# Optimization experiments

Hardware: AMD Instinct MI355X
Metric: run time of the kernel (lower is better)

## Reference

```python
import jax, jax.numpy as jnp
import numpy as np

N_NODES = 2048
D = 1024
B = 16384
E = 65536

def setup_inputs() -> dict:
    key = jax.random.key(0)
    ks = jax.random.split(key, 8)
    feat = jax.random.normal(ks[0], (B, 7, D), dtype=jnp.float32)
    data_x = jax.random.randint(ks[1], (7 * B,), 0, N_NODES, dtype=jnp.int64)
    adj_rows = jnp.sort(jax.random.randint(ks[2], (E,), 0, N_NODES, dtype=jnp.int32))
    adj_cols = jax.random.randint(ks[3], (E,), 0, N_NODES, dtype=jnp.int32)
    adj_vals = jax.random.uniform(ks[4], (E,), dtype=jnp.float32)
    # kaiming-uniform-like init for GCN weights, zero bias (as in reset_parameters)
    def kaiming(k, fan_in, fan_out):
        bound = jnp.sqrt(6.0 / fan_in)
        return jax.random.uniform(k, (fan_in, fan_out), minval=-bound, maxval=bound, dtype=jnp.float32)
    W1 = kaiming(ks[5], D, N_NODES)
    W2 = kaiming(ks[6], N_NODES, N_NODES)
    W3 = kaiming(ks[7], N_NODES, D)
    return {"feat": feat, "data_x": data_x, "adj_rows": adj_rows, "adj_cols": adj_cols,
            "adj_vals": adj_vals, "W1": W1, "b1": jnp.zeros((N_NODES,), jnp.float32),
            "W2": W2, "b2": jnp.zeros((N_NODES,), jnp.float32),
            "W3": W3, "b3": jnp.zeros((D,), jnp.float32)}

def reference(feat, data_x, adj_rows, adj_cols, adj_vals, W1, b1, W2, b2, W3, b3):
    n = b1.shape[0]  # number of nodes N
    e1 = data_x[0::7]  # [B]
    e2 = data_x[1::7]  # [B]
    # scatter-add: adjacency_matrix[e1] += feat[i,0]; adjacency_matrix[e2] += feat[i,1]
    idx = jnp.concatenate([e1, e2])                       # [2B]
    vals = jnp.concatenate([feat[:, 0, :], feat[:, 1, :]])  # [2B, D]
    node_feat = jax.ops.segment_sum(vals, idx, num_segments=n)  # [N, D]

    def spmm(x):  # sparse [N,N] @ dense [N,F]
        return jax.ops.segment_sum(adj_vals[:, None] * x[adj_cols], adj_rows, num_segments=n)

    h = jax.nn.relu(spmm(node_feat @ W1) + b1)  # [N, N]
    h = spmm(h @ W2) + b2                        # [N, N]
    logits = spmm(h @ W3) + b3                   # [N, D]

    # gather then swap: feat[:,0]=logits[e2], feat[:,1]=logits[e1]
    out = jnp.concatenate([logits[e2][:, None, :], logits[e1][:, None, :], feat[:, 2:, :]], axis=1)
    return out
```

## Files before the change

### kernel.cpp

```cpp
#include <hip/hip_runtime.h>
#include <stdint.h>

#define N_NODES 2048
#define DIM 1024
#define BATCH 16384
#define NEDGE 65536
#define CAP 96

typedef __bf16 bf16x8 __attribute__((ext_vector_type(8)));
typedef float f32x4 __attribute__((ext_vector_type(4)));
typedef unsigned short u16;
typedef unsigned int u32;

__device__ __forceinline__ float bf2f(u16 u) {
  union { u32 i; float f; } v; v.i = ((u32)u) << 16; return v.f;
}
__device__ __forceinline__ u16 f2bf(float f) {
  union { float f; u32 i; } v; v.f = f;
  u32 r = v.i + 0x7fffu + ((v.i >> 16) & 1u);
  return (u16)(r >> 16);
}

__global__ void k_detect(const int* __restrict__ dx, int* __restrict__ flag,
                         int* __restrict__ counts) {
  int t = threadIdx.x;
  for (int j = t; j < N_NODES; j += 64) counts[j] = 0;
  if (t == 0) {
    int is64 = 1;
    for (int j = 0; j < 32; ++j)
      if (dx[2 * j + 1] != 0) { is64 = 0; break; }
    *flag = is64;
  }
}

__global__ __launch_bounds__(256) void k_cvt(const int* __restrict__ dx,
                                             const int* __restrict__ flag,
                                             int* __restrict__ idx) {
  int i = blockIdx.x * 256 + threadIdx.x;
  if (i >= 7 * BATCH) return;
  int v = (*flag) ? dx[2 * i] : dx[i];
  idx[i] = v & (N_NODES - 1);
}

__global__ __launch_bounds__(256) void k_bucket(const int* __restrict__ idx,
                                                int* __restrict__ counts,
                                                int* __restrict__ bucket) {
  int i = blockIdx.x * 256 + threadIdx.x;
  if (i >= 2 * BATCH) return;
  int n = (i < BATCH) ? idx[7 * i] : idx[7 * (i - BATCH) + 1];
  int slot = atomicAdd(&counts[n], 1);
  if (slot < CAP) bucket[n * CAP + slot] = i;
}

__global__ __launch_bounds__(256) void k_nodesum(const float* __restrict__ feat,
                                                 const int* __restrict__ counts,
                                                 const int* __restrict__ bucket,
                                                 u16* __restrict__ A1) {
  int n = blockIdx.x;
  int tid = threadIdx.x;
  int cnt = counts[n]; if (cnt > CAP) cnt = CAP;
  float a0 = 0.f, a1 = 0.f, a2 = 0.f, a3 = 0.f;
  for (int j = 0; j < cnt; ++j) {
    int i = bucket[n * CAP + j];
    size_t rowoff = (i < BATCH) ? ((size_t)i * 7) * DIM
                                : ((size_t)(i - BATCH) * 7 + 1) * DIM;
    f32x4 v = *(const f32x4*)(feat + rowoff + tid * 4);
    a0 += v[0]; a1 += v[1]; a2 += v[2]; a3 += v[3];
  }
  ushort4 o; o.x = f2bf(a0); o.y = f2bf(a1); o.z = f2bf(a2); o.w = f2bf(a3);
  *(ushort4*)(A1 + (size_t)n * DIM + tid * 4) = o;
}

__global__ __launch_bounds__(256) void k_transpose(const float* __restrict__ W,
                                                   u16* __restrict__ Wt,
                                                   int K, int N) {
  __shared__ __align__(16) u16 t[32][33];
  int ntx = N >> 5;
  int bx = blockIdx.x % ntx;
  int by = blockIdx.x / ntx;
  int tx = threadIdx.x & 31, ty = threadIdx.x >> 5;
  #pragma unroll
  for (int r = 0; r < 32; r += 8)
    t[r + ty][tx] = f2bf(W[(size_t)(by * 32 + r + ty) * N + bx * 32 + tx]);
  __syncthreads();
  #pragma unroll
  for (int r = 0; r < 32; r += 8)
    Wt[(size_t)(bx * 32 + r + ty) * K + by * 32 + tx] = t[tx][r + ty];
}

__global__ __launch_bounds__(256) void k_rowptr(const int* __restrict__ adj_rows,
                                                int* __restrict__ row_ptr) {
  int r = blockIdx.x * 256 + threadIdx.x;
  if (r > N_NODES) return;
  int lo = 0, hi = NEDGE;
  while (lo < hi) { int mid = (lo + hi) >> 1; if (adj_rows[mid] < r) lo = mid + 1; else hi = mid; }
  row_ptr[r] = lo;
}

__global__ __launch_bounds__(256) void k_spmm(const u16* __restrict__ X16,
                                              const int* __restrict__ row_ptr,
                                              const int* __restrict__ adj_cols,
                                              const float* __restrict__ adj_vals,
                                              const float* __restrict__ bias,
                                              u16* __restrict__ Y16,
                                              float* __restrict__ Y32,
                                              int width) {
  int chunks = width >> 10;
  int ch = blockIdx.x % chunks;
  int r = blockIdx.x / chunks;
  int col = ch * 1024 + threadIdx.x * 4;
  int e0 = row_ptr[r], e1 = row_ptr[r + 1];
  float a0 = 0.f, a1 = 0.f, a2 = 0.f, a3 = 0.f;
  for (int e = e0; e < e1; ++e) {
    int c = adj_cols[e] & (N_NODES - 1);
    float v = adj_vals[e];
    ushort4 x = *(const ushort4*)(X16 + (size_t)c * width + col);
    a0 += v * bf2f(x.x); a1 += v * bf2f(x.y);
    a2 += v * bf2f(x.z); a3 += v * bf2f(x.w);
  }
  if (Y16) {
    ushort4 o; o.x = f2bf(a0); o.y = f2bf(a1); o.z = f2bf(a2); o.w = f2bf(a3);
    *(ushort4*)(Y16 + (size_t)r * width + col) = o;
  } else {
    f32x4 bb = *(const f32x4*)(bias + col);
    f32x4 o; o[0] = a0 + bb[0]; o[1] = a1 + bb[1]; o[2] = a2 + bb[2]; o[3] = a3 + bb[3];
    *(f32x4*)(Y32 + (size_t)r * width + col) = o;
  }
}

template <int BM, int BN, bool BIAS, bool RELU>
__global__ __launch_bounds__(256) void k_gemm(const u16* __restrict__ A,
                                              const u16* __restrict__ Bt,
                                              const float* __restrict__ bias,
                                              u16* __restrict__ C16,
                                              int M, int N, int K) {
  constexpr int WM = BM / 2, WN = BN / 2;
  constexpr int MI = WM / 16, NI = WN / 16;
  constexpr int IA = BM / 64, IB = BN / 64;
  __shared__ __align__(16) u16 As[BM * 32];
  __shared__ __align__(16) u16 Bs[BN * 32];
  const int ntx = N / BN;
  const int bx = blockIdx.x % ntx;
  const int by = blockIdx.x / ntx;
  const int tid = threadIdx.x;
  const int wid = tid >> 6;
  const int lane = tid & 63;
  const int wr = wid >> 1, wc = wid & 1;
  const int rowbase = by * BM, colbase = bx * BN;

  f32x4 acc[MI][NI];
  #pragma unroll
  for (int i = 0; i < MI; ++i)
    #pragma unroll
    for (int j = 0; j < NI; ++j) acc[i][j] = (f32x4){0.f, 0.f, 0.f, 0.f};

  const int srow = wid * 16 + (lane >> 2);
  const int skk = (lane & 3) * 8;

  for (int kt = 0; kt < K; kt += 32) {
    #pragma unroll
    for (int i = 0; i < IA; ++i) {
      const u16* g = A + (size_t)(rowbase + i * 64 + srow) * K + kt + skk;
      __builtin_amdgcn_global_load_lds(
          (const __attribute__((address_space(1))) u32*)g,
          (__attribute__((address_space(3))) u32*)(As + i * 2048 + wid * 512), 16, 0, 0);
    }
    #pragma unroll
    for (int i = 0; i < IB; ++i) {
      const u16* g = Bt + (size_t)(colbase + i * 64 + srow) * K + kt + skk;
      __builtin_amdgcn_global_load_lds(
          (const __attribute__((address_space(1))) u32*)g,
          (__attribute__((address_space(3))) u32*)(Bs + i * 2048 + wid * 512), 16, 0, 0);
    }
    __syncthreads();
    bf16x8 af[MI], bfr[NI];
    #pragma unroll
    for (int mi = 0; mi < MI; ++mi) {
      int row = wr * WM + mi * 16 + (lane & 15);
      af[mi] = *(const bf16x8*)(As + row * 32 + (lane >> 4) * 8);
    }
    #pragma unroll
    for (int ni = 0; ni < NI; ++ni) {
      int col = wc * WN + ni * 16 + (lane & 15);
      bfr[ni] = *(const bf16x8*)(Bs + col * 32 + (lane >> 4) * 8);
    }
    #pragma unroll
    for (int mi = 0; mi < MI; ++mi)
      #pragma unroll
      for (int ni = 0; ni < NI; ++ni)
        acc[mi][ni] = __builtin_amdgcn_mfma_f32_16x16x32_bf16(af[mi], bfr[ni], acc[mi][ni], 0, 0, 0);
    __syncthreads();
  }

  #pragma unroll
  for (int mi = 0; mi < MI; ++mi) {
    #pragma unroll
    for (int ni = 0; ni < NI; ++ni) {
      int col = colbase + wc * WN + ni * 16 + (lane & 15);
      float bv = BIAS ? bias[col] : 0.f;
      #pragma unroll
      for (int j = 0; j < 4; ++j) {
        int row = rowbase + wr * WM + mi * 16 + (lane >> 4) * 4 + j;
        float v = acc[mi][ni][j] + bv;
        if (RELU) v = fmaxf(v, 0.f);
        C16[(size_t)row * N + col] = f2bf(v);
      }
    }
  }
}

__global__ __launch_bounds__(256) void k_assemble(const float* __restrict__ feat,
                                                  const float* __restrict__ logits,
                                                  const int* __restrict__ idx,
                                                  float* __restrict__ out) {
  int i = blockIdx.x;
  int b = i / 7, slot = i - b * 7;
  const float* src;
  if (slot == 0)      src = logits + (size_t)idx[7 * b + 1] * DIM;
  else if (slot == 1) src = logits + (size_t)idx[7 * b] * DIM;
  else                src = feat + ((size_t)b * 7 + slot) * DIM;
  f32x4 v = *(const f32x4*)(src + threadIdx.x * 4);
  __builtin_nontemporal_store(v, (f32x4*)(out + ((size_t)b * 7 + slot) * DIM + threadIdx.x * 4));
}

extern "C" void kernel_launch(void* const* d_in, const int* in_sizes, int n_in,
                              void* d_out, int out_size, void* d_ws, size_t ws_size,
                              hipStream_t stream) {
  const float* feat   = (const float*)d_in[0];
  const int* data_x   = (const int*)d_in[1];
  const int* adj_rows = (const int*)d_in[2];
  const int* adj_cols = (const int*)d_in[3];
  const float* adj_vals = (const float*)d_in[4];
  const float* W1 = (const float*)d_in[5];
  const float* b1 = (const float*)d_in[6];
  const float* W2 = (const float*)d_in[7];
  const float* b2 = (const float*)d_in[8];
  const float* W3 = (const float*)d_in[9];
  const float* b3 = (const float*)d_in[10];
  float* out = (float*)d_out;

  char* ws = (char*)d_ws;
  size_t off = 0;
  auto alloc = [&](size_t bytes) {
    char* p = ws + off; off += (bytes + 511) & ~(size_t)511; return p;
  };
  int*  flag    = (int*)alloc(4);
  int*  idx32   = (int*)alloc((size_t)7 * BATCH * 4);
  int*  counts  = (int*)alloc(N_NODES * 4);
  int*  bucket  = (int*)alloc((size_t)N_NODES * CAP * 4);
  int*  row_ptr = (int*)alloc((N_NODES + 1) * 4);
  u16*  A1      = (u16*)alloc((size_t)N_NODES * DIM * 2);
  u16*  S       = (u16*)alloc((size_t)N_NODES * N_NODES * 2);
  u16*  H       = (u16*)alloc((size_t)N_NODES * N_NODES * 2);
  u16*  X3      = (u16*)alloc((size_t)N_NODES * DIM * 2);
  u16*  Wt      = (u16*)alloc((size_t)N_NODES * N_NODES * 2);
  float* logits = (float*)alloc((size_t)N_NODES * DIM * 4);

  k_detect<<<1, 64, 0, stream>>>(data_x, flag, counts);
  k_cvt<<<(7 * BATCH + 255) / 256, 256, 0, stream>>>(data_x, flag, idx32);
  k_bucket<<<(2 * BATCH + 255) / 256, 256, 0, stream>>>(idx32, counts, bucket);
  k_nodesum<<<N_NODES, 256, 0, stream>>>(feat, counts, bucket, A1);
  k_rowptr<<<N_NODES / 256 + 1, 256, 0, stream>>>(adj_rows, row_ptr);

  k_transpose<<<(N_NODES / 32) * (DIM / 32), 256, 0, stream>>>(W1, Wt, DIM, N_NODES);
  k_spmm<<<N_NODES * (DIM / 1024), 256, 0, stream>>>(A1, row_ptr, adj_cols, adj_vals, nullptr, S, nullptr, DIM);
  k_gemm<128, 64, true, true><<<(N_NODES / 128) * (N_NODES / 64), 256, 0, stream>>>(S, Wt, b1, H, N_NODES, N_NODES, DIM);
  k_transpose<<<(N_NODES / 32) * (N_NODES / 32), 256, 0, stream>>>(W2, Wt, N_NODES, N_NODES);
  k_spmm<<<N_NODES * (N_NODES / 1024), 256, 0, stream>>>(H, row_ptr, adj_cols, adj_vals, nullptr, S, nullptr, N_NODES);
  k_gemm<128, 64, true, false><<<(N_NODES / 128) * (N_NODES / 64), 256, 0, stream>>>(S, Wt, b2, H, N_NODES, N_NODES, N_NODES);
  k_transpose<<<(DIM / 32) * (N_NODES / 32), 256, 0, stream>>>(W3, Wt, N_NODES, DIM);
  k_gemm<64, 64, false, false><<<(N_NODES / 64) * (DIM / 64), 256, 0, stream>>>(H, Wt, nullptr, X3, N_NODES, DIM, N_NODES);
  k_spmm<<<N_NODES * (DIM / 1024), 256, 0, stream>>>(X3, row_ptr, adj_cols, adj_vals, b3, nullptr, logits, DIM);

  k_assemble<<<BATCH * 7, 256, 0, stream>>>(feat, logits, idx32, out);
}
```

Baseline: 354.1 us.

## Double-buffer GEMM with BK=64 swizzled LDS, unroll SpMM, drop index conversion kernel

The GEMM moves to a 64-wide K tile with double-buffered LDS, prefetching the next tile while MFMAs run on the current one. An XOR swizzle on LDS addresses is meant to avoid bank conflicts. The SpMM edge loop is unrolled by two so more gather loads are in flight at once. The separate index-conversion kernel is removed, and k_bucket and k_assemble now read data_x directly with the 64-bit flag, saving one launch and an intermediate buffer. The cost is doubled LDS use, which may reduce occupancy.

```diff
diff --git a/kernel.cpp b/kernel.cpp
--- a/kernel.cpp
+++ b/kernel.cpp
@@ -33,21 +33,15 @@
   }
 }
 
-__global__ __launch_bounds__(256) void k_cvt(const int* __restrict__ dx,
-                                             const int* __restrict__ flag,
-                                             int* __restrict__ idx) {
-  int i = blockIdx.x * 256 + threadIdx.x;
-  if (i >= 7 * BATCH) return;
-  int v = (*flag) ? dx[2 * i] : dx[i];
-  idx[i] = v & (N_NODES - 1);
-}
-
-__global__ __launch_bounds__(256) void k_bucket(const int* __restrict__ idx,
+__global__ __launch_bounds__(256) void k_bucket(const int* __restrict__ dx,
+                                                const int* __restrict__ flag,
                                                 int* __restrict__ counts,
                                                 int* __restrict__ bucket) {
   int i = blockIdx.x * 256 + threadIdx.x;
   if (i >= 2 * BATCH) return;
-  int n = (i < BATCH) ? idx[7 * i] : idx[7 * (i - BATCH) + 1];
+  int f = *flag;
+  long p = (i < BATCH) ? 7L * i : 7L * (i - BATCH) + 1;
+  int n = dx[f ? 2 * p : p] & (N_NODES - 1);
   int slot = atomicAdd(&counts[n], 1);
   if (slot < CAP) bucket[n * CAP + slot] = i;
 }
@@ -111,7 +105,19 @@
   int col = ch * 1024 + threadIdx.x * 4;
   int e0 = row_ptr[r], e1 = row_ptr[r + 1];
   float a0 = 0.f, a1 = 0.f, a2 = 0.f, a3 = 0.f;
-  for (int e = e0; e < e1; ++e) {
+  int e = e0;
+  for (; e + 2 <= e1; e += 2) {
+    int c0 = adj_cols[e] & (N_NODES - 1);
+    int c1 = adj_cols[e + 1] & (N_NODES - 1);
+    float v0 = adj_vals[e], v1 = adj_vals[e + 1];
+    ushort4 x0 = *(const ushort4*)(X16 + (size_t)c0 * width + col);
+    ushort4 x1 = *(const ushort4*)(X16 + (size_t)c1 * width + col);
+    a0 += v0 * bf2f(x0.x) + v1 * bf2f(x1.x);
+    a1 += v0 * bf2f(x0.y) + v1 * bf2f(x1.y);
+    a2 += v0 * bf2f(x0.z) + v1 * bf2f(x1.z);
+    a3 += v0 * bf2f(x0.w) + v1 * bf2f(x1.w);
+  }
+  if (e < e1) {
     int c = adj_cols[e] & (N_NODES - 1);
     float v = adj_vals[e];
     ushort4 x = *(const ushort4*)(X16 + (size_t)c * width + col);
@@ -134,11 +140,12 @@
                                               const float* __restrict__ bias,
                                               u16* __restrict__ C16,
                                               int M, int N, int K) {
+  constexpr int BK = 64;
   constexpr int WM = BM / 2, WN = BN / 2;
   constexpr int MI = WM / 16, NI = WN / 16;
-  constexpr int IA = BM / 64, IB = BN / 64;
-  __shared__ __align__(16) u16 As[BM * 32];
-  __shared__ __align__(16) u16 Bs[BN * 32];
+  constexpr int IA = BM / 32, IB = BN / 32;
+  __shared__ __align__(16) u16 As[2][BM * BK];
+  __shared__ __align__(16) u16 Bs[2][BN * BK];
   const int ntx = N / BN;
   const int bx = blockIdx.x % ntx;
   const int by = blockIdx.x / ntx;
@@ -154,49 +161,72 @@
     #pragma unroll
     for (int j = 0; j < NI; ++j) acc[i][j] = (f32x4){0.f, 0.f, 0.f, 0.f};
 
-  const int srow = wid * 16 + (lane >> 2);
-  const int skk = (lane & 3) * 8;
-
-  for (int kt = 0; kt < K; kt += 32) {
-    #pragma unroll
-    for (int i = 0; i < IA; ++i) {
-      const u16* g = A + (size_t)(rowbase + i * 64 + srow) * K + kt + skk;
-      __builtin_amdgcn_global_load_lds(
-          (const __attribute__((address_space(1))) u32*)g,
-          (__attribute__((address_space(3))) u32*)(As + i * 2048 + wid * 512), 16, 0, 0);
+  const int srow = tid >> 3;
+  const int skk = (((tid & 7) ^ (srow & 7)) << 3);
+
+  #define STAGE(buf, kt)                                                        \
+    do {                                                                        \
+      _Pragma("unroll")                                                         \
+      for (int i = 0; i < IA; ++i) {                                            \
+        const u16* g = A + (size_t)(rowbase + i * 32 + srow) * K + (kt) + skk;  \
+        __builtin_amdgcn_global_load_lds(                                       \
+            (const __attribute__((address_space(1))) u32*)g,                    \
+            (__attribute__((address_space(3))) u32*)(&As[buf][i * 2048 + tid * 8]), \
+            16, 0, 0);                                                          \
+      }                                                                         \
+      _Pragma("unroll")                                                         \
+      for (int i = 0; i < IB; ++i) {                                            \
+        const u16* g = Bt + (size_t)(colbase + i * 32 + srow) * K + (kt) + skk; \
+        __builtin_amdgcn_global_load_lds(                                       \
+            (const __attribute__((address_space(1))) u32*)g,                    \
+            (__attribute__((address_space(3))) u32*)(&Bs[buf][i * 2048 + tid * 8]), \
+            16, 0, 0);                                                          \
+      }                                                                         \
+    } while (0)
+
+  const int rrow = lane & 15;
+  const int kq = (lane >> 4) * 8;
+  const int rswz = (lane & 7) << 3;
+
+  const int nk = K >> 6;
+  STAGE(0, 0);
+  __syncthreads();
+
+  for (int t = 0; t < nk; ++t) {
+    const u16* as = As[t & 1];
+    const u16* bs = Bs[t & 1];
+    if (t + 1 < nk) STAGE((t + 1) & 1, (t + 1) << 6);
+    bf16x8 af[MI][2], bfr[NI][2];
+    #pragma unroll
+    for (int mi = 0; mi < MI; ++mi) {
+      int r = wr * WM + mi * 16 + rrow;
+      #pragma unroll
+      for (int h = 0; h < 2; ++h)
+        af[mi][h] = *(const bf16x8*)(as + r * 64 + ((h * 32 + kq) ^ rswz));
     }
     #pragma unroll
-    for (int i = 0; i < IB; ++i) {
-      const u16* g = Bt + (size_t)(colbase + i * 64 + srow) * K + kt + skk;
-      __builtin_amdgcn_global_load_lds(
-          (const __attribute__((address_space(1))) u32*)g,
-          (__attribute__((address_space(3))) u32*)(Bs + i * 2048 + wid * 512), 16, 0, 0);
+    for (int ni = 0; ni < NI; ++ni) {
+      int c = wc * WN + ni * 16 + rrow;
+      #pragma unroll
+      for (int h = 0; h < 2; ++h)
+        bfr[ni][h] = *(const bf16x8*)(bs + c * 64 + ((h * 32 + kq) ^ rswz));
     }
+    #pragma unroll
+    for (int h = 0; h < 2; ++h)
+      #pragma unroll
+      for (int mi = 0; mi < MI; ++mi)
+        #pragma unroll
+        for (int ni = 0; ni < NI; ++ni)
+          acc[mi][ni] = __builtin_amdgcn_mfma_f32_16x16x32_bf16(af[mi][h], bfr[ni][h], acc[mi][ni], 0, 0, 0);
     __syncthreads();
-    bf16x8 af[MI], bfr[NI];
-    #pragma unroll
-    for (int mi = 0; mi < MI; ++mi) {
-      int row = wr * WM + mi * 16 + (lane & 15);
-      af[mi] = *(const bf16x8*)(As + row * 32 + (lane >> 4) * 8);
-    }
-    #pragma unroll
-    for (int ni = 0; ni < NI; ++ni) {
-      int col = wc * WN + ni * 16 + (lane & 15);
-      bfr[ni] = *(const bf16x8*)(Bs + col * 32 + (lane >> 4) * 8);
-    }
-    #pragma unroll
-    for (int mi = 0; mi < MI; ++mi)
-      #pragma unroll
-      for (int ni = 0; ni < NI; ++ni)
-        acc[mi][ni] = __builtin_amdgcn_mfma_f32_16x16x32_bf16(af[mi], bfr[ni], acc[mi][ni], 0, 0, 0);
-    __syncthreads();
-  }
+  }
+  #undef STAGE
 
   #pragma unroll
   for (int mi = 0; mi < MI; ++mi) {
     #pragma unroll
     for (int ni = 0; ni < NI; ++ni) {
-      int col = colbase + wc * WN + ni * 16 + (lane & 15);
+      int col = colbase + wc * WN + ni * 16 + rrow;
       float bv = BIAS ? bias[col] : 0.f;
       #pragma unroll
       for (int j = 0; j < 4; ++j) {
@@ -211,14 +241,20 @@
 
 __global__ __launch_bounds__(256) void k_assemble(const float* __restrict__ feat,
                                                   const float* __restrict__ logits,
-                                                  const int* __restrict__ idx,
+                                                  const int* __restrict__ dx,
+                                                  const int* __restrict__ flag,
                                                   float* __restrict__ out) {
   int i = blockIdx.x;
   int b = i / 7, slot = i - b * 7;
   const float* src;
-  if (slot == 0)      src = logits + (size_t)idx[7 * b + 1] * DIM;
-  else if (slot == 1) src = logits + (size_t)idx[7 * b] * DIM;
-  else                src = feat + ((size_t)b * 7 + slot) * DIM;
+  if (slot <= 1) {
+    int f = *flag;
+    long p = 7L * b + (slot == 0 ? 1 : 0);
+    int node = dx[f ? 2 * p : p] & (N_NODES - 1);
+    src = logits + (size_t)node * DIM;
+  } else {
+    src = feat + ((size_t)b * 7 + slot) * DIM;
+  }
   f32x4 v = *(const f32x4*)(src + threadIdx.x * 4);
   __builtin_nontemporal_store(v, (f32x4*)(out + ((size_t)b * 7 + slot) * DIM + threadIdx.x * 4));
 }
@@ -245,7 +281,6 @@
     char* p = ws + off; off += (bytes + 511) & ~(size_t)511; return p;
   };
   int*  flag    = (int*)alloc(4);
-  int*  idx32   = (int*)alloc((size_t)7 * BATCH * 4);
   int*  counts  = (int*)alloc(N_NODES * 4);
   int*  bucket  = (int*)alloc((size_t)N_NODES * CAP * 4);
   int*  row_ptr = (int*)alloc((N_NODES + 1) * 4);
@@ -257,8 +292,7 @@
   float* logits = (float*)alloc((size_t)N_NODES * DIM * 4);
 
   k_detect<<<1, 64, 0, stream>>>(data_x, flag, counts);
-  k_cvt<<<(7 * BATCH + 255) / 256, 256, 0, stream>>>(data_x, flag, idx32);
-  k_bucket<<<(2 * BATCH + 255) / 256, 256, 0, stream>>>(idx32, counts, bucket);
+  k_bucket<<<(2 * BATCH + 255) / 256, 256, 0, stream>>>(data_x, flag, counts, bucket);
   k_nodesum<<<N_NODES, 256, 0, stream>>>(feat, counts, bucket, A1);
   k_rowptr<<<N_NODES / 256 + 1, 256, 0, stream>>>(adj_rows, row_ptr);
 
@@ -272,5 +306,5 @@
   k_gemm<64, 64, false, false><<<(N_NODES / 64) * (DIM / 64), 256, 0, stream>>>(H, Wt, nullptr, X3, N_NODES, DIM, N_NODES);
   k_spmm<<<N_NODES * (DIM / 1024), 256, 0, stream>>>(X3, row_ptr, adj_cols, adj_vals, b3, nullptr, logits, DIM);
 
-  k_assemble<<<BATCH * 7, 256, 0, stream>>>(feat, logits, idx32, out);
-}
+  k_assemble<<<BATCH * 7, 256, 0, stream>>>(feat, logits, data_x, flag, out);
+}
```

Result: faster. 322.9 us (-8.8%).
